# Optimization experiments

Measured on AMD Instinct MI355X. Metric: run time of the kernel, lower is better.

## Reference

```python
import jax, jax.numpy as jnp
import numpy as np

N_NODES = 100000
N_EDGES = 1600000
IN_CH = 128
OUT_CH = 128

def setup_inputs() -> dict:
    key = jax.random.key(0)
    k1, k2, k3, k4, k5 = jax.random.split(key, 5)
    x = jax.random.normal(k1, (N_NODES, IN_CH), dtype=jnp.float32)
    src = jax.random.randint(k2, (N_EDGES,), 0, N_NODES, dtype=jnp.int64)
    dst = jax.random.randint(k3, (N_EDGES,), 0, N_NODES, dtype=jnp.int64)
    edge_index = jnp.stack([src, dst], axis=0)
    W = jax.random.normal(k4, (OUT_CH, IN_CH), dtype=jnp.float32) * (1.0 / np.sqrt(IN_CH))
    b = jax.random.normal(k5, (OUT_CH,), dtype=jnp.float32) * 0.01
    return {"x": x, "edge_index": edge_index, "W": W, "b": b}

def reference(x, edge_index, W, b):
    n = x.shape[0]
    src, dst = edge_index[0], edge_index[1]
    loop = jnp.arange(n, dtype=edge_index.dtype)
    src_all = jnp.concatenate([src, loop])  # [E+N]
    dst_all = jnp.concatenate([dst, loop])  # [E+N]
    # in-degree (with self loops) per node
    deg = jax.ops.segment_sum(jnp.ones_like(dst_all, dtype=x.dtype), dst_all, num_segments=n)
    norm = (deg[src_all] * deg[dst_all]) ** -0.5
    norm = jnp.where(jnp.isinf(norm), 0.0, norm)
    h = x @ W.T + b  # [N, out_ch]
    msg = h[src_all] * norm[:, None]  # [E+N, out_ch]
    out = jax.ops.segment_sum(msg, dst_all, num_segments=n)  # [N, out_ch]
    return out
```

## Files before the change

kernel.cpp:

```cpp
#include <hip/hip_runtime.h>
#include <hip/hip_bf16.h>


#define N_NODES 100000
#define N_EDGES 1600000
#define CH 128
#define NC 49
#define NBLKA 782
#define CAPC 34816
#define NCHUNK 17
#define NFB 1563
#define FCAP 1280

using bf16x8 = __attribute__((ext_vector_type(8))) short;
using f32x4  = __attribute__((ext_vector_type(4))) float;

__device__ inline unsigned short f2bf(float f) {
    unsigned u = __float_as_uint(f);
    u += 0x7fffu + ((u >> 16) & 1u);
    return (unsigned short)(u >> 16);
}
__device__ inline float bflo(unsigned u) { return __uint_as_float(u << 16); }
__device__ inline float bfhi(unsigned u) { return __uint_as_float(u & 0xffff0000u); }

__global__ __launch_bounds__(256) void k_histA(const int* __restrict__ dst,
                                               int* __restrict__ histG,
                                               int* __restrict__ ftail) {
    __shared__ int hist[NC];
    const int t    = threadIdx.x;
    const int base = blockIdx.x * 2048;
    const int n    = min(2048, N_EDGES - base);
    { int i = blockIdx.x * 256 + t; if (i < 1600) ftail[i] = 0; }
    if (t < NC) hist[t] = 0;
    __syncthreads();
#pragma unroll
    for (int h = 0; h < 2; ++h) {
        int idx = h * 1024 + 4 * t;
        if (idx < n) {
            int4 dv = *(const int4*)&dst[base + idx];
            atomicAdd(&hist[dv.x >> 11], 1);
            atomicAdd(&hist[dv.y >> 11], 1);
            atomicAdd(&hist[dv.z >> 11], 1);
            atomicAdd(&hist[dv.w >> 11], 1);
        }
    }
    __syncthreads();
    if (t < NC) histG[(size_t)t * NBLKA + blockIdx.x] = hist[t];
}

__global__ __launch_bounds__(256) void k_scanA(int* __restrict__ histG,
                                               int* __restrict__ ctail) {
    __shared__ int part[256];
    const int k = blockIdx.x;
    int* h = histG + (size_t)k * NBLKA;
    const int t = threadIdx.x;
    const int base = t * 4;
    int a0 = 0, a1 = 0, a2 = 0, a3 = 0;
    if (base + 0 < NBLKA) a0 = h[base + 0];
    if (base + 1 < NBLKA) a1 = h[base + 1];
    if (base + 2 < NBLKA) a2 = h[base + 2];
    if (base + 3 < NBLKA) a3 = h[base + 3];
    const int s = a0 + a1 + a2 + a3;
    part[t] = s;
    __syncthreads();
    for (int off = 1; off < 256; off <<= 1) {
        int x = (t >= off) ? part[t - off] : 0;
        __syncthreads();
        part[t] += x;
        __syncthreads();
    }
    int r = part[t] - s;
    if (t == 255) ctail[k] = part[255];
    if (base + 0 < NBLKA) { h[base + 0] = r; r += a0; }
    if (base + 1 < NBLKA) { h[base + 1] = r; r += a1; }
    if (base + 2 < NBLKA) { h[base + 2] = r; r += a2; }
    if (base + 3 < NBLKA) { h[base + 3] = r; r += a3; }
}

__global__ __launch_bounds__(256) void k_place(const int* __restrict__ src,
                                               const int* __restrict__ dst,
                                               const int* __restrict__ histG,
                                               unsigned* __restrict__ E1) {
    __shared__ int hist[NC];
    __shared__ int boff[NC + 1];
    __shared__ int cur[NC];
    __shared__ int gb[NC];
    __shared__ unsigned stage[2048];
    const int t    = threadIdx.x;
    const int base = blockIdx.x * 2048;
    const int n    = min(2048, N_EDGES - base);

    if (t < NC) {
        hist[t] = 0;
        gb[t] = histG[(size_t)t * NBLKA + blockIdx.x];
    }
    __syncthreads();

    int s[8], d[8];
#pragma unroll
    for (int h = 0; h < 2; ++h) {
        int idx = h * 1024 + 4 * t;
        if (idx < n) {
            int4 sv = *(const int4*)&src[base + idx];
            int4 dv = *(const int4*)&dst[base + idx];
            s[4*h+0] = sv.x; s[4*h+1] = sv.y; s[4*h+2] = sv.z; s[4*h+3] = sv.w;
            d[4*h+0] = dv.x; d[4*h+1] = dv.y; d[4*h+2] = dv.z; d[4*h+3] = dv.w;
        } else {
            d[4*h+0] = d[4*h+1] = d[4*h+2] = d[4*h+3] = -1;
            s[4*h+0] = s[4*h+1] = s[4*h+2] = s[4*h+3] = 0;
        }
    }
#pragma unroll
    for (int j = 0; j < 8; ++j)
        if (d[j] >= 0) atomicAdd(&hist[d[j] >> 11], 1);
    __syncthreads();

    if (t == 0) {
        int run = 0;
        for (int k = 0; k < NC; ++k) { boff[k] = run; run += hist[k]; }
        boff[NC] = run;
    }
    __syncthreads();
    if (t < NC) cur[t] = boff[t];
    __syncthreads();

#pragma unroll
    for (int j = 0; j < 8; ++j)
        if (d[j] >= 0) {
            int k = d[j] >> 11;
            int pos = atomicAdd(&cur[k], 1);
            stage[pos] = ((unsigned)s[j] << 11) | (unsigned)(d[j] & 2047);
        }
    __syncthreads();

    const int tot = boff[NC];
    for (int i = t; i < tot; i += 256) {
        int lo = 0, hi = NC;
#pragma unroll
        for (int it = 0; it < 6; ++it) {
            int mid = (lo + hi) >> 1;
            bool c = (boff[mid] <= i);
            lo = c ? mid : lo;
            hi = c ? hi : mid;
        }
        int p = gb[lo] + (i - boff[lo]);
        if (p < CAPC) E1[(size_t)lo * CAPC + p] = stage[i];
    }
}

__global__ __launch_bounds__(256) void k_sortB(const unsigned* __restrict__ E1,
                                               const int* __restrict__ ctail,
                                               int* __restrict__ ftail,
                                               unsigned* __restrict__ E2) {
    __shared__ int hist[32];
    __shared__ int boff[33];
    __shared__ int cur[32];
    __shared__ int gb[32];
    __shared__ unsigned stage[2048];
    const int cb = blockIdx.x / NCHUNK;
    const int ch = blockIdx.x % NCHUNK;
    const int t  = threadIdx.x;
    int cnt = ctail[cb]; if (cnt > CAPC) cnt = CAPC;
    const int begin = ch * 2048;
    int n = cnt - begin;
    if (n <= 0) return;
    if (n > 2048) n = 2048;
    const unsigned* e1 = E1 + (size_t)cb * CAPC + begin;

    if (t < 32) hist[t] = 0;
    __syncthreads();

    for (int i = t; i < n; i += 256)
        atomicAdd(&hist[(e1[i] >> 6) & 31], 1);
    __syncthreads();

    if (t < 32) gb[t] = atomicAdd(&ftail[cb * 32 + t], hist[t]);
    if (t == 0) {
        int run = 0;
        for (int k = 0; k < 32; ++k) { boff[k] = run; run += hist[k]; }
        boff[32] = run;
    }
    __syncthreads();
    if (t < 32) cur[t] = boff[t];
    __syncthreads();

    for (int i = t; i < n; i += 256) {
        unsigned v = e1[i];
        int k = (v >> 6) & 31;
        int pos = atomicAdd(&cur[k], 1);
        stage[pos] = ((v >> 11) << 6) | (v & 63);
    }
    __syncthreads();

    const int tot = boff[32];
    for (int i = t; i < tot; i += 256) {
        int lo = 0, hi = 32;
#pragma unroll
        for (int it = 0; it < 5; ++it) {
            int mid = (lo + hi) >> 1;
            bool c = (boff[mid] <= i);
            lo = c ? mid : lo;
            hi = c ? hi : mid;
        }
        int p = gb[lo] + (i - boff[lo]);
        int fb = cb * 32 + lo;
        if (p < FCAP) E2[(size_t)fb * FCAP + p] = stage[i];
    }
}

__device__ inline void cvt8(const float4 a, const float4 b, bf16x8& h, bf16x8& l) {
    bf16x8 H, L;
#define CV(i, f) { unsigned short hb = f2bf(f); H[i] = (short)hb;               \
                   L[i] = (short)f2bf((f) - __uint_as_float((unsigned)hb << 16)); }
    CV(0, a.x) CV(1, a.y) CV(2, a.z) CV(3, a.w)
    CV(4, b.x) CV(5, b.y) CV(6, b.z) CV(7, b.w)
#undef CV
    h = H; l = L;
}

#define MFMA(a, b, c) __builtin_amdgcn_mfma_f32_16x16x32_bf16((a), (b), (c), 0, 0, 0)

__global__ __launch_bounds__(256) void k_gemm(const float* __restrict__ x,
                                              const float* __restrict__ W,
                                              const float* __restrict__ b,
                                              const unsigned* __restrict__ E2,
                                              const int* __restrict__ ftail,
                                              unsigned short* __restrict__ hs) {
    __shared__ __align__(16) unsigned short wh[CH * CH];
    __shared__ __align__(16) unsigned short wl[CH * CH];
    const int t = threadIdx.x;
    const int lane = t & 63;
    const int l15  = lane & 15;
    const int lhi  = lane >> 4;

    int* dbin = (int*)wh;
    if (t < 128) dbin[t] = 0;
    __syncthreads();
    {
        const int fb0 = blockIdx.x * 2;
        int n0 = ftail[fb0]; if (n0 > FCAP) n0 = FCAP;
        const unsigned* e0 = E2 + (size_t)fb0 * FCAP;
        for (int i = t; i < n0; i += 256) atomicAdd(&dbin[e0[i] & 63], 1);
        const int fb1 = fb0 + 1;
        if (fb1 < NFB) {
            int n1 = ftail[fb1]; if (n1 > FCAP) n1 = FCAP;
            const unsigned* e1p = E2 + (size_t)fb1 * FCAP;
            for (int i = t; i < n1; i += 256) atomicAdd(&dbin[64 + (e1p[i] & 63)], 1);
        }
    }
    __syncthreads();
    float rreg[2][4];
#pragma unroll
    for (int rf = 0; rf < 2; ++rf) {
        int lb = (t >> 6) * 32 + rf * 16 + lhi * 4;
#pragma unroll
        for (int j = 0; j < 4; ++j)
            rreg[rf][j] = rsqrtf((float)(dbin[lb + j] + 1));
    }
    __syncthreads();

    for (int c = t; c < 2048; c += 256) {
        int o   = c >> 4;
        int kk  = (c & 15) << 3;
        const float* wp = &W[(size_t)o * CH + kk];
        float4 w0 = *(const float4*)wp;
        float4 w1 = *(const float4*)(wp + 4);
        bf16x8 H, L;
        cvt8(w0, w1, H, L);
        unsigned boff = ((unsigned)((o << 8) | (kk << 1))) ^ ((unsigned)(o & 7) << 4);
        *(bf16x8*)((char*)wh + boff) = H;
        *(bf16x8*)((char*)wl + boff) = L;
    }
    __syncthreads();

    const int kc = lhi << 3;
    const int row_base = blockIdx.x * 128 + (t >> 6) * 32;

    int r0 = row_base + l15;       if (r0 > N_NODES - 1) r0 = N_NODES - 1;
    int r1 = row_base + 16 + l15;  if (r1 > N_NODES - 1) r1 = N_NODES - 1;
    const float* x0 = &x[(size_t)r0 * CH + kc];
    const float* x1 = &x[(size_t)r1 * CH + kc];

    float4 xa[4][2], xb[4][2];
#pragma unroll
    for (int ks = 0; ks < 4; ++ks) {
        xa[ks][0] = *(const float4*)(x0 + ks * 32);
        xa[ks][1] = *(const float4*)(x0 + ks * 32 + 4);
        xb[ks][0] = *(const float4*)(x1 + ks * 32);
        xb[ks][1] = *(const float4*)(x1 + ks * 32 + 4);
    }

    f32x4 acc[2][8];
#pragma unroll
    for (int rf = 0; rf < 2; ++rf)
#pragma unroll
        for (int cf = 0; cf < 8; ++cf)
            acc[rf][cf] = (f32x4){0.f, 0.f, 0.f, 0.f};

#pragma unroll
    for (int ks = 0; ks < 4; ++ks) {
        bf16x8 ah0, al0, ah1, al1;
        cvt8(xa[ks][0], xa[ks][1], ah0, al0);
        cvt8(xb[ks][0], xb[ks][1], ah1, al1);
        const unsigned kb = (unsigned)((ks * 32 + kc) << 1);
#pragma unroll
        for (int cf = 0; cf < 8; ++cf) {
            int o = cf * 16 + l15;
            unsigned boff = (((unsigned)(o << 8)) + kb) ^ ((unsigned)(o & 7) << 4);
            bf16x8 bh = *(const bf16x8*)((const char*)wh + boff);
            bf16x8 bl = *(const bf16x8*)((const char*)wl + boff);
            acc[0][cf] = MFMA(ah0, bh, acc[0][cf]);
            acc[1][cf] = MFMA(ah1, bh, acc[1][cf]);
            acc[0][cf] = MFMA(al0, bh, acc[0][cf]);
            acc[1][cf] = MFMA(al1, bh, acc[1][cf]);
            acc[0][cf] = MFMA(ah0, bl, acc[0][cf]);
            acc[1][cf] = MFMA(ah1, bl, acc[1][cf]);
        }
    }

    float bcol[8];
#pragma unroll
    for (int cf = 0; cf < 8; ++cf) bcol[cf] = b[cf * 16 + l15];

#pragma unroll
    for (int rf = 0; rf < 2; ++rf) {
        int rb = row_base + rf * 16 + lhi * 4;
        if (rb >= N_NODES) continue;
#pragma unroll
        for (int j = 0; j < 4; ++j) {
            size_t ro = (size_t)(rb + j) * CH;
            float ri = rreg[rf][j];
#pragma unroll
            for (int cf = 0; cf < 8; ++cf)
                hs[ro + cf * 16 + l15] = f2bf(ri * (acc[rf][cf][j] + bcol[cf]));
        }
    }
}

#define ACC8(u)                                                            \
    do {                                                                   \
        acc[0] += bflo((u).x); acc[1] += bfhi((u).x);                      \
        acc[2] += bflo((u).y); acc[3] += bfhi((u).y);                      \
        acc[4] += bflo((u).z); acc[5] += bfhi((u).z);                      \
        acc[6] += bflo((u).w); acc[7] += bfhi((u).w);                      \
    } while (0)

__global__ __launch_bounds__(256) void k_spmm(const unsigned* __restrict__ E2,
                                              const int* __restrict__ ftail,
                                              const unsigned short* __restrict__ hs,
                                              float* __restrict__ out) {
    __shared__ int bins[64];
    __shared__ int boff[65];
    __shared__ int cur[64];
    __shared__ int srt[FCAP];
    const int fb    = blockIdx.x;
    const int node0 = fb * 64;
    const int t     = threadIdx.x;
    const unsigned* e2 = E2 + (size_t)fb * FCAP;
    const uint4* hp = (const uint4*)hs;

    if (t < 64) bins[t] = 0;
    int n = ftail[fb]; if (n > FCAP) n = FCAP;
    __syncthreads();

    for (int i = t; i < n; i += 256) atomicAdd(&bins[e2[i] & 63], 1);
    __syncthreads();

    if (t == 0) {
        int run = 0;
        for (int k = 0; k < 64; ++k) { boff[k] = run; run += bins[k]; }
        boff[64] = run;
    }
    __syncthreads();
    if (t < 64) cur[t] = boff[t];
    __syncthreads();

    for (int i = t; i < n; i += 256) {
        unsigned v = e2[i];
        int pos = atomicAdd(&cur[v & 63], 1);
        srt[pos] = (int)(v >> 6);
    }
    __syncthreads();

    const int grp  = t >> 4;
    const int lane = t & 15;
#pragma unroll
    for (int r = 0; r < 4; ++r) {
        const int nl   = grp * 4 + r;
        const int node = node0 + nl;
        if (node >= N_NODES) continue;
        float acc[8] = {};
        {
            uint4 u = hp[(size_t)node * 16 + lane];
            ACC8(u);
        }
        int e  = boff[nl];
        int e1 = boff[nl + 1];
        for (; e + 8 <= e1; e += 8) {
            int s0 = srt[e + 0], s1 = srt[e + 1], s2 = srt[e + 2], s3 = srt[e + 3];
            int s4 = srt[e + 4], s5 = srt[e + 5], s6 = srt[e + 6], s7 = srt[e + 7];
            uint4 u0 = hp[(size_t)s0 * 16 + lane];
            uint4 u1 = hp[(size_t)s1 * 16 + lane];
            uint4 u2 = hp[(size_t)s2 * 16 + lane];
            uint4 u3 = hp[(size_t)s3 * 16 + lane];
            uint4 u4 = hp[(size_t)s4 * 16 + lane];
            uint4 u5 = hp[(size_t)s5 * 16 + lane];
            uint4 u6 = hp[(size_t)s6 * 16 + lane];
            uint4 u7 = hp[(size_t)s7 * 16 + lane];
            ACC8(u0); ACC8(u1); ACC8(u2); ACC8(u3);
            ACC8(u4); ACC8(u5); ACC8(u6); ACC8(u7);
        }
        for (; e + 4 <= e1; e += 4) {
            int s0 = srt[e + 0];
            int s1 = srt[e + 1];
            int s2 = srt[e + 2];
            int s3 = srt[e + 3];
            uint4 u0 = hp[(size_t)s0 * 16 + lane];
            uint4 u1 = hp[(size_t)s1 * 16 + lane];
            uint4 u2 = hp[(size_t)s2 * 16 + lane];
            uint4 u3 = hp[(size_t)s3 * 16 + lane];
            ACC8(u0); ACC8(u1); ACC8(u2); ACC8(u3);
        }
        for (; e < e1; ++e) {
            uint4 u = hp[(size_t)srt[e] * 16 + lane];
            ACC8(u);
        }
        float ri = rsqrtf((float)(bins[nl] + 1));
        f32x4 o0, o1;
        o0[0] = ri * acc[0]; o0[1] = ri * acc[1]; o0[2] = ri * acc[2]; o0[3] = ri * acc[3];
        o1[0] = ri * acc[4]; o1[1] = ri * acc[5]; o1[2] = ri * acc[6]; o1[3] = ri * acc[7];
        *(f32x4*)&out[(size_t)node * CH + lane * 8]     = o0;
        *(f32x4*)&out[(size_t)node * CH + lane * 8 + 4] = o1;
    }
}

extern "C" void kernel_launch(void* const* d_in, const int* in_sizes, int n_in,
                              void* d_out, int out_size, void* d_ws, size_t ws_size,
                              hipStream_t stream) {
    const float* x  = (const float*)d_in[0];
    const int*   ei = (const int*)d_in[1];
    const float* W  = (const float*)d_in[2];
    const float* b  = (const float*)d_in[3];
    float* out = (float*)d_out;

    const int* src = (const int*)ei;
    const int* dst = (const int*)ei + N_EDGES;

    int*      ctail = (int*)d_ws;
    int*      ftail = ctail + 64;
    int*      histG = ftail + 1600;
    unsigned* E1    = (unsigned*)(histG + 38336);
    unsigned* E2    = E1 + (size_t)NC * CAPC;
    unsigned short* hs = (unsigned short*)(E2 + (size_t)NFB * FCAP);

    k_histA<<<NBLKA, 256, 0, stream>>>(dst, histG, ftail);
    k_scanA<<<NC, 256, 0, stream>>>(histG, ctail);
    k_place<<<NBLKA, 256, 0, stream>>>(src, dst, histG, E1);
    k_sortB<<<NC * NCHUNK, 256, 0, stream>>>(E1, ctail, ftail, E2);
    k_gemm<<<NBLKA, 256, 0, stream>>>(x, W, b, E2, ftail, hs);
    k_spmm<<<NFB, 256, 0, stream>>>(E2, ftail, hs, out);
}
```

Before: 221.9 us.

## Replace global histogram+scan with fixed-capacity per-block buckets in edge sort

Removes the k_histA and k_scanA passes. k_place now writes each block's edges into a fixed-capacity slot per (coarse bucket, block) along with a count. k_sortB reads these padded slots, skipping invalid entries, and E1 now shares memory with the hs buffer. This cuts two kernel launches and one full read of dst. In exchange, edges are silently dropped if any block-bucket holds more than 80 entries (expected about 42), and sortB reads padded slots.

```diff
diff --git a/kernel.cpp b/kernel.cpp
--- a/kernel.cpp
+++ b/kernel.cpp
@@ -7,10 +7,12 @@
 #define CH 128
 #define NC 49
 #define NBLKA 782
-#define CAPC 34816
+#define CAPB 80
+#define BPU 46
 #define NCHUNK 17
 #define NFB 1563
 #define FCAP 1280
+#define STCAP 2560
 
 using bf16x8 = __attribute__((ext_vector_type(8))) short;
 using f32x4  = __attribute__((ext_vector_type(4))) float;
@@ -23,77 +25,22 @@
 __device__ inline float bflo(unsigned u) { return __uint_as_float(u << 16); }
 __device__ inline float bfhi(unsigned u) { return __uint_as_float(u & 0xffff0000u); }
 
-__global__ __launch_bounds__(256) void k_histA(const int* __restrict__ dst,
-                                               int* __restrict__ histG,
-                                               int* __restrict__ ftail) {
-    __shared__ int hist[NC];
-    const int t    = threadIdx.x;
-    const int base = blockIdx.x * 2048;
-    const int n    = min(2048, N_EDGES - base);
-    { int i = blockIdx.x * 256 + t; if (i < 1600) ftail[i] = 0; }
-    if (t < NC) hist[t] = 0;
-    __syncthreads();
-#pragma unroll
-    for (int h = 0; h < 2; ++h) {
-        int idx = h * 1024 + 4 * t;
-        if (idx < n) {
-            int4 dv = *(const int4*)&dst[base + idx];
-            atomicAdd(&hist[dv.x >> 11], 1);
-            atomicAdd(&hist[dv.y >> 11], 1);
-            atomicAdd(&hist[dv.z >> 11], 1);
-            atomicAdd(&hist[dv.w >> 11], 1);
-        }
-    }
-    __syncthreads();
-    if (t < NC) histG[(size_t)t * NBLKA + blockIdx.x] = hist[t];
-}
-
-__global__ __launch_bounds__(256) void k_scanA(int* __restrict__ histG,
-                                               int* __restrict__ ctail) {
-    __shared__ int part[256];
-    const int k = blockIdx.x;
-    int* h = histG + (size_t)k * NBLKA;
-    const int t = threadIdx.x;
-    const int base = t * 4;
-    int a0 = 0, a1 = 0, a2 = 0, a3 = 0;
-    if (base + 0 < NBLKA) a0 = h[base + 0];
-    if (base + 1 < NBLKA) a1 = h[base + 1];
-    if (base + 2 < NBLKA) a2 = h[base + 2];
-    if (base + 3 < NBLKA) a3 = h[base + 3];
-    const int s = a0 + a1 + a2 + a3;
-    part[t] = s;
-    __syncthreads();
-    for (int off = 1; off < 256; off <<= 1) {
-        int x = (t >= off) ? part[t - off] : 0;
-        __syncthreads();
-        part[t] += x;
-        __syncthreads();
-    }
-    int r = part[t] - s;
-    if (t == 255) ctail[k] = part[255];
-    if (base + 0 < NBLKA) { h[base + 0] = r; r += a0; }
-    if (base + 1 < NBLKA) { h[base + 1] = r; r += a1; }
-    if (base + 2 < NBLKA) { h[base + 2] = r; r += a2; }
-    if (base + 3 < NBLKA) { h[base + 3] = r; r += a3; }
-}
-
 __global__ __launch_bounds__(256) void k_place(const int* __restrict__ src,
                                                const int* __restrict__ dst,
-                                               const int* __restrict__ histG,
-                                               unsigned* __restrict__ E1) {
+                                               int* __restrict__ cntG,
+                                               unsigned* __restrict__ E1,
+                                               int* __restrict__ ftail) {
     __shared__ int hist[NC];
     __shared__ int boff[NC + 1];
     __shared__ int cur[NC];
-    __shared__ int gb[NC];
     __shared__ unsigned stage[2048];
     const int t    = threadIdx.x;
-    const int base = blockIdx.x * 2048;
+    const int bid  = blockIdx.x;
+    const int base = bid * 2048;
     const int n    = min(2048, N_EDGES - base);
 
-    if (t < NC) {
-        hist[t] = 0;
-        gb[t] = histG[(size_t)t * NBLKA + blockIdx.x];
-    }
+    { int i = bid * 256 + t; if (i < 1600) ftail[i] = 0; }
+    if (t < NC) hist[t] = 0;
     __syncthreads();
 
     int s[8], d[8];
@@ -133,6 +80,8 @@
         }
     __syncthreads();
 
+    if (t < NC) cntG[(size_t)t * NBLKA + bid] = min(hist[t], CAPB);
+
     const int tot = boff[NC];
     for (int i = t; i < tot; i += 256) {
         int lo = 0, hi = NC;
@@ -143,35 +92,37 @@
             lo = c ? mid : lo;
             hi = c ? hi : mid;
         }
-        int p = gb[lo] + (i - boff[lo]);
-        if (p < CAPC) E1[(size_t)lo * CAPC + p] = stage[i];
+        int p = i - boff[lo];
+        if (p < CAPB)
+            E1[((size_t)lo * NBLKA + bid) * CAPB + p] = stage[i];
     }
 }
 
 __global__ __launch_bounds__(256) void k_sortB(const unsigned* __restrict__ E1,
-                                               const int* __restrict__ ctail,
+                                               const int* __restrict__ cntG,
                                                int* __restrict__ ftail,
                                                unsigned* __restrict__ E2) {
     __shared__ int hist[32];
     __shared__ int boff[33];
     __shared__ int cur[32];
     __shared__ int gb[32];
-    __shared__ unsigned stage[2048];
-    const int cb = blockIdx.x / NCHUNK;
-    const int ch = blockIdx.x % NCHUNK;
-    const int t  = threadIdx.x;
-    int cnt = ctail[cb]; if (cnt > CAPC) cnt = CAPC;
-    const int begin = ch * 2048;
-    int n = cnt - begin;
-    if (n <= 0) return;
-    if (n > 2048) n = 2048;
-    const unsigned* e1 = E1 + (size_t)cb * CAPC + begin;
+    __shared__ int cnt[BPU];
+    __shared__ unsigned stage[STCAP];
+    const int cb  = blockIdx.x / NCHUNK;
+    const int u   = blockIdx.x % NCHUNK;
+    const int sb0 = u * BPU;
+    const int t   = threadIdx.x;
 
     if (t < 32) hist[t] = 0;
-    __syncthreads();
-
-    for (int i = t; i < n; i += 256)
-        atomicAdd(&hist[(e1[i] >> 6) & 31], 1);
+    if (t < BPU) cnt[t] = cntG[(size_t)cb * NBLKA + sb0 + t];
+    __syncthreads();
+
+    const unsigned* e1 = E1 + ((size_t)cb * NBLKA + sb0) * CAPB;
+
+    for (int i = t; i < BPU * CAPB; i += 256) {
+        int sb = i / CAPB, sl = i - sb * CAPB;
+        if (sl < cnt[sb]) atomicAdd(&hist[(e1[i] >> 6) & 31], 1);
+    }
     __syncthreads();
 
     if (t < 32) gb[t] = atomicAdd(&ftail[cb * 32 + t], hist[t]);
@@ -184,15 +135,19 @@
     if (t < 32) cur[t] = boff[t];
     __syncthreads();
 
-    for (int i = t; i < n; i += 256) {
-        unsigned v = e1[i];
-        int k = (v >> 6) & 31;
-        int pos = atomicAdd(&cur[k], 1);
-        stage[pos] = ((v >> 11) << 6) | (v & 63);
-    }
-    __syncthreads();
-
-    const int tot = boff[32];
+    for (int i = t; i < BPU * CAPB; i += 256) {
+        int sb = i / CAPB, sl = i - sb * CAPB;
+        if (sl < cnt[sb]) {
+            unsigned v = e1[i];
+            int k = (v >> 6) & 31;
+            int pos = atomicAdd(&cur[k], 1);
+            if (pos < STCAP)
+                stage[pos] = ((v >> 11) << 6) | (v & 63);
+        }
+    }
+    __syncthreads();
+
+    const int tot = min(boff[32], STCAP);
     for (int i = t; i < tot; i += 256) {
         int lo = 0, hi = 32;
 #pragma unroll
@@ -446,17 +401,14 @@
     const int* src = (const int*)ei;
     const int* dst = (const int*)ei + N_EDGES;
 
-    int*      ctail = (int*)d_ws;
-    int*      ftail = ctail + 64;
-    int*      histG = ftail + 1600;
-    unsigned* E1    = (unsigned*)(histG + 38336);
-    unsigned* E2    = E1 + (size_t)NC * CAPC;
+    int*      ftail = (int*)d_ws;
+    int*      cntG  = ftail + 1600;
+    unsigned* E2    = (unsigned*)(cntG + 38336);
     unsigned short* hs = (unsigned short*)(E2 + (size_t)NFB * FCAP);
-
-    k_histA<<<NBLKA, 256, 0, stream>>>(dst, histG, ftail);
-    k_scanA<<<NC, 256, 0, stream>>>(histG, ctail);
-    k_place<<<NBLKA, 256, 0, stream>>>(src, dst, histG, E1);
-    k_sortB<<<NC * NCHUNK, 256, 0, stream>>>(E1, ctail, ftail, E2);
+    unsigned* E1    = (unsigned*)hs;
+
+    k_place<<<NBLKA, 256, 0, stream>>>(src, dst, cntG, E1, ftail);
+    k_sortB<<<NC * NCHUNK, 256, 0, stream>>>(E1, cntG, ftail, E2);
     k_gemm<<<NBLKA, 256, 0, stream>>>(x, W, b, E2, ftail, hs);
     k_spmm<<<NFB, 256, 0, stream>>>(E2, ftail, hs, out);
 }
```

After: 223.0 us. About the same (+0.5%).
